# Performance work log

Hardware: AMD Instinct MI355X
Metric: run time of the kernel (lower is better)

Reference implementation:

```python
import jax, jax.numpy as jnp
import numpy as np

PATCH = 3
PAD = (PATCH - 1) // 2
WEIGHT = 100.0
EPS = 1e-9


def _extract_patches(fm):
    # fm: (C, H, W) -> (H*W, C*9) row i*W+j is the reflect-padded 3x3 patch at (i, j)
    C, H, W = fm.shape
    fm_pad = jnp.pad(fm, ((0, 0), (PAD, PAD), (PAD, PAD)), mode='reflect')
    shifts = [fm_pad[:, dh:dh + H, dw:dw + W] for dh in range(PATCH) for dw in range(PATCH)]
    p = jnp.stack(shifts, axis=0)            # (9, C, H, W)
    return p.reshape(PATCH * PATCH * C, H * W).T  # (HW, 9C)


def _match_fm(content_fm, style_fm):
    # content_fm, style_fm: (1, C, H, W); returns matched style fm (1,C,H,W) and idx (2,H,W)
    C, H, W = content_fm.shape[1:]
    cp = _extract_patches(content_fm[0])     # (HW, 9C) content patches (conv kernels)
    sp = _extract_patches(style_fm[0])       # (HW, 9C) style patches (conv sliding windows)
    c_norm = jnp.sqrt(jnp.sum(cp * cp, axis=1))  # kernel_norm per content location
    s_norm = jnp.sqrt(jnp.sum(sp * sp, axis=1))  # style_fm_norm per style location
    score = cp @ sp.T                            # (HW, HW) cross-correlation
    score = score / (c_norm[:, None] * s_norm[None, :] + EPS)
    idx = jnp.argmax(score, axis=1)              # flat argmax == torch.argmax on (H,W) map
    style_flat = style_fm[0].reshape(C, H * W)
    corr = style_flat[:, idx].reshape(1, C, H, W)  # gather matched style pixels
    corr_idx = jnp.stack([idx // W, idx % W], axis=0).reshape(2, H, W)
    return corr, corr_idx


def _masked_gram(fm, mask_flat, mask_sum):
    # fm: (1, C, H, W), mask_flat: (HW,) -> (C, C) gram of masked fm / sum(mask)
    C = fm.shape[1]
    f = fm[0].reshape(C, -1) * mask_flat[None, :]
    return (f @ f.T) / mask_sum


def setup_inputs() -> dict:
    key = jax.random.key(0)
    k1, k2, k3, k4 = jax.random.split(key, 4)
    B, C, H, W = 1, 512, 64, 64
    return {
        'content_fm': jax.random.normal(k1, (B, C, H, W), dtype=jnp.float32),
        'style_fm': jax.random.normal(k2, (B, C, H, W), dtype=jnp.float32),
        'input_fm': jax.random.normal(k3, (B, C, H, W), dtype=jnp.float32),
        'mask': jax.random.uniform(k4, (B, 1, H, W), dtype=jnp.float32),
    }


def reference(content_fm, style_fm, input_fm, mask):
    H, W = content_fm.shape[2:]
    mask_flat = mask[0, 0].reshape(H * W)
    mask_sum = jnp.sum(mask)
    # capture_style_ref: patch-match style fm to content fm, build target gram
    corr_fm, _ = _match_fm(content_fm, style_fm)
    target_gram = _masked_gram(corr_fm, mask_flat, mask_sum)
    # loss mode: masked gram of current image fm vs target, MSE (mean) * weight
    G = _masked_gram(input_fm, mask_flat, mask_sum)
    loss = jnp.mean((G - target_gram) ** 2) * WEIGHT
    return loss
```

## Files before the change

kernel.cpp:

```cpp
#include <hip/hip_runtime.h>

static constexpr int C  = 512;
static constexpr int P  = 4096;
static constexpr int CC = 262144;

typedef _Float16 half8  __attribute__((ext_vector_type(8)));
typedef _Float16 half2v __attribute__((ext_vector_type(2)));
typedef float    f32x4  __attribute__((ext_vector_type(4)));

__device__ __forceinline__ int refl(int q) { return q < 0 ? 1 : (q > 63 ? 62 : q); }

__device__ __forceinline__ void g2l16(const void* g, const void* l) {
    __builtin_amdgcn_global_load_lds((const __attribute__((address_space(1))) unsigned int*)g,
                                     (__attribute__((address_space(3))) unsigned int*)l, 16, 0, 0);
}

__global__ void k_init(float* __restrict__ small) {
    int e = blockIdx.x * 256 + threadIdx.x;
    if (e < 4096) small[e] = 0.0f;
    if (e == 0) small[8193] = 0.0f;
}

__global__ __launch_bounds__(256) void k_prep(const float* __restrict__ content, const float* __restrict__ style,
                                              _Float16* __restrict__ Ah, _Float16* __restrict__ Bh,
                                              float* __restrict__ sqn_s) {
    __shared__ float T[64][65];
    const int p0 = (blockIdx.x & 63) * 64, c0 = (blockIdx.x >> 6) * 64;
    const int pl = threadIdx.x & 63, cq = threadIdx.x >> 6;
    const int cl2 = threadIdx.x & 63, pq = threadIdx.x >> 6;

    #pragma unroll
    for (int r = 0; r < 16; ++r) {
        int cl = cq + r * 4;
        T[cl][pl] = content[(size_t)(c0 + cl) * P + p0 + pl];
    }
    __syncthreads();
    #pragma unroll
    for (int r = 0; r < 16; ++r) {
        int pl2 = pq + r * 4;
        Ah[(size_t)(p0 + pl2) * C + c0 + cl2] = (_Float16)T[cl2][pl2];
    }
    __syncthreads();

    float sq = 0.f;
    #pragma unroll
    for (int r = 0; r < 16; ++r) {
        int cl = cq + r * 4;
        float v = style[(size_t)(c0 + cl) * P + p0 + pl];
        T[cl][pl] = v;
        sq += v * v;
    }
    atomicAdd(&sqn_s[p0 + pl], sq);
    __syncthreads();
    #pragma unroll
    for (int r = 0; r < 16; ++r) {
        int pl2 = pq + r * 4;
        Bh[(size_t)(p0 + pl2) * C + c0 + cl2] = (_Float16)T[cl2][pl2];
    }
}

__global__ void k_pnorm(const float* __restrict__ sqn_s, const float* __restrict__ mask,
                        float* __restrict__ inv_sn, float* __restrict__ msum) {
    int p = blockIdx.x * 256 + threadIdx.x;
    int i = p >> 6, j = p & 63;
    float s2 = 0.f;
    #pragma unroll
    for (int dh = -1; dh <= 1; ++dh) {
        int ih = refl(i + dh);
        #pragma unroll
        for (int dw = -1; dw <= 1; ++dw)
            s2 += sqn_s[ih * 64 + refl(j + dw)];
    }
    inv_sn[p] = 1.0f / sqrtf(s2);

    if (blockIdx.x == 0) {
        __shared__ float red[256];
        float s = 0.f;
        for (int e = threadIdx.x; e < P; e += 256) s += mask[e];
        red[threadIdx.x] = s;
        __syncthreads();
        for (int t = 128; t > 0; t >>= 1) {
            if (threadIdx.x < t) red[threadIdx.x] += red[threadIdx.x + t];
            __syncthreads();
        }
        if (threadIdx.x == 0) msum[0] = red[0];
    }
}

__global__ __launch_bounds__(256) void k_gemm16(const _Float16* __restrict__ Ah,
                                                const _Float16* __restrict__ Bh,
                                                _Float16* __restrict__ Eo) {
    __shared__ _Float16 SH[16640];
    _Float16* As = SH;
    _Float16* Bs = SH + 8192;
    const int tid = threadIdx.x;
    const int wave = tid >> 6, lane = tid & 63;
    const int wr = wave >> 1, wc = wave & 1;
    const int quad = lane >> 4, l15 = lane & 15;
    const int i0 = blockIdx.y * 128, j0 = blockIdx.x * 128;

    int mloc[4], goff[4];
    #pragma unroll
    for (int c2 = 0; c2 < 4; ++c2) {
        int m = wave * 32 + c2 * 8 + (lane >> 3);
        mloc[c2] = m;
        goff[c2] = ((lane & 7) ^ (m & 7)) * 8;
    }

    int aoff[4][2], boff[4][2];
    #pragma unroll
    for (int mi = 0; mi < 4; ++mi) {
        int m = wr * 64 + mi * 16 + l15;
        int n = wc * 64 + mi * 16 + l15;
        #pragma unroll
        for (int kh = 0; kh < 2; ++kh) {
            aoff[mi][kh] = m * 64 + ((quad + kh * 4) ^ (m & 7)) * 8;
            boff[mi][kh] = n * 64 + ((quad + kh * 4) ^ (n & 7)) * 8;
        }
    }

    f32x4 acc[4][4] = {};

    for (int kk = 0; kk < C; kk += 64) {
        __syncthreads();
        #pragma unroll
        for (int c2 = 0; c2 < 4; ++c2) {
            g2l16(Ah + (size_t)(i0 + mloc[c2]) * C + kk + goff[c2], As + (wave * 32 + c2 * 8) * 64);
            g2l16(Bh + (size_t)(j0 + mloc[c2]) * C + kk + goff[c2], Bs + (wave * 32 + c2 * 8) * 64);
        }
        __syncthreads();
        half8 af[2][4], bf[2][4];
        #pragma unroll
        for (int kh = 0; kh < 2; ++kh)
            #pragma unroll
            for (int mi = 0; mi < 4; ++mi) {
                af[kh][mi] = *(const half8*)(As + aoff[mi][kh]);
                bf[kh][mi] = *(const half8*)(Bs + boff[mi][kh]);
            }
        #pragma unroll
        for (int kh = 0; kh < 2; ++kh)
            #pragma unroll
            for (int mi = 0; mi < 4; ++mi)
                #pragma unroll
                for (int ni = 0; ni < 4; ++ni)
                    acc[mi][ni] = __builtin_amdgcn_mfma_f32_16x16x32_f16(af[kh][mi], bf[kh][ni], acc[mi][ni], 0, 0, 0);
    }

    __syncthreads();
    #pragma unroll
    for (int mi = 0; mi < 4; ++mi) {
        int row = wr * 64 + mi * 16 + quad * 4;
        #pragma unroll
        for (int ni = 0; ni < 4; ++ni) {
            int col = wc * 64 + ni * 16 + l15;
            #pragma unroll
            for (int r = 0; r < 4; ++r)
                SH[(row + r) * 130 + col] = (_Float16)acc[mi][ni][r];
        }
    }
    __syncthreads();

    const int er  = tid >> 1;
    const int ec0 = (tid & 1) << 6;
    const int aw = er & 63;
    const int rm = (er & 64) | (aw == 0 ? 1 : aw - 1);
    const int rp = (er & 64) | (aw == 63 ? 62 : aw + 1);
    _Float16* outRow = Eo + (size_t)(i0 + er) * P + j0 + ec0;
    #pragma unroll
    for (int cc = 0; cc < 64; cc += 8) {
        half8 ev;
        #pragma unroll
        for (int u = 0; u < 8; ++u) {
            int c = ec0 + cc + u;
            int cw = c & 63;
            int cm = (c & 64) | (cw == 0 ? 1 : cw - 1);
            int cp = (c & 64) | (cw == 63 ? 62 : cw + 1);
            ev[u] = (_Float16)((float)SH[rm * 130 + cm] + (float)SH[er * 130 + c] + (float)SH[rp * 130 + cp]);
        }
        *(half8*)(outRow + cc) = ev;
    }
}

__global__ __launch_bounds__(256) void k_argmax(const _Float16* __restrict__ E,
                                                const float* __restrict__ inv_sn,
                                                int* __restrict__ idxOut) {
    const int i = blockIdx.x;
    const int ih = i >> 6, iw = i & 63;
    const int wave = threadIdx.x >> 6, l = threadIdx.x & 63, l15 = l & 15;
    size_t rb0 = (size_t)(refl(ih - 1) * 64 + iw) * P;
    size_t rb1 = (size_t)(ih * 64 + iw) * P;
    size_t rb2 = (size_t)(refl(ih + 1) * 64 + iw) * P;

    float best = -1e30f;
    int bidx = 0;
    #pragma unroll
    for (int s = 0; s < 4; ++s) {
        const int j0 = (wave * 4 + s) * 256 + l * 4;
        const int jh = j0 >> 6, jw0 = l15 * 4;
        const int cb0 = ((jh == 0) ? 1 : jh - 1) * 64 + jw0;
        const int cb1 = jh * 64 + jw0;
        const int cb2 = ((jh == 63) ? 62 : jh + 1) * 64 + jw0;
        uint2 u0 = *(const uint2*)(E + rb0 + cb0);
        uint2 u1 = *(const uint2*)(E + rb1 + cb1);
        uint2 u2 = *(const uint2*)(E + rb2 + cb2);
        half2v a0 = __builtin_bit_cast(half2v, u0.x), a1 = __builtin_bit_cast(half2v, u0.y);
        half2v b0 = __builtin_bit_cast(half2v, u1.x), b1 = __builtin_bit_cast(half2v, u1.y);
        half2v c0 = __builtin_bit_cast(half2v, u2.x), c1 = __builtin_bit_cast(half2v, u2.y);
        float f0 = (float)a0[0] + (float)b0[0] + (float)c0[0];
        float f1 = (float)a0[1] + (float)b0[1] + (float)c0[1];
        float f2 = (float)a1[0] + (float)b1[0] + (float)c1[0];
        float f3 = (float)a1[1] + (float)b1[1] + (float)c1[1];
        const float4 is = *(const float4*)(inv_sn + j0);
        float v0 = f0 * is.x, v1 = f1 * is.y, v2 = f2 * is.z, v3 = f3 * is.w;
        if (v0 > best) { best = v0; bidx = j0; }
        if (v1 > best) { best = v1; bidx = j0 + 1; }
        if (v2 > best) { best = v2; bidx = j0 + 2; }
        if (v3 > best) { best = v3; bidx = j0 + 3; }
    }

    __shared__ float bv[256];
    __shared__ int   bi[256];
    bv[threadIdx.x] = best;
    bi[threadIdx.x] = bidx;
    __syncthreads();
    for (int t = 128; t > 0; t >>= 1) {
        if (threadIdx.x < t) {
            float ov = bv[threadIdx.x + t];
            int   oi = bi[threadIdx.x + t];
            if (ov > bv[threadIdx.x] || (ov == bv[threadIdx.x] && oi < bi[threadIdx.x])) {
                bv[threadIdx.x] = ov;
                bi[threadIdx.x] = oi;
            }
        }
        __syncthreads();
    }
    if (threadIdx.x == 0) idxOut[i] = bi[0];
}

__global__ void k_build(const float* __restrict__ style, const float* __restrict__ input,
                        const float* __restrict__ mask, const int* __restrict__ idx,
                        _Float16* __restrict__ fc, _Float16* __restrict__ fg) {
    int t = blockIdx.x * 256 + threadIdx.x;
    int e0 = t * 8;
    int p0 = e0 & (P - 1), c = e0 >> 12;
    half8 vg, vc;
    #pragma unroll
    for (int u = 0; u < 8; ++u) {
        float m = mask[p0 + u];
        vg[u] = (_Float16)(input[e0 + u] * m);
        vc[u] = (_Float16)(style[(c << 12) + idx[p0 + u]] * m);
    }
    *(half8*)(fg + e0) = vg;
    *(half8*)(fc + e0) = vc;
}

__global__ __launch_bounds__(256) void k_gram(const _Float16* __restrict__ fg,
                                              const _Float16* __restrict__ fc,
                                              float* __restrict__ part) {
    const int z = blockIdx.z;
    const int p0 = z * 256;
    const int wave = threadIdx.x >> 6, lane = threadIdx.x & 63;
    const int wr = wave >> 1, wc = wave & 1, quad = lane >> 4, l15 = lane & 15;
    const int a0 = blockIdx.y * 128 + wr * 64, b0 = blockIdx.x * 128 + wc * 64;

    f32x4 accg[4][4] = {};
    f32x4 accc[4][4] = {};
    for (int ks = 0; ks < 256; ks += 32) {
        int kbase = p0 + ks + quad * 8;
        half8 af[4], bf[4];
        #pragma unroll
        for (int mi = 0; mi < 4; ++mi) af[mi] = *(const half8*)(fg + (size_t)(a0 + mi * 16 + l15) * P + kbase);
        #pragma unroll
        for (int ni = 0; ni < 4; ++ni) bf[ni] = *(const half8*)(fg + (size_t)(b0 + ni * 16 + l15) * P + kbase);
        #pragma unroll
        for (int mi = 0; mi < 4; ++mi)
            #pragma unroll
            for (int ni = 0; ni < 4; ++ni)
                accg[mi][ni] = __builtin_amdgcn_mfma_f32_16x16x32_f16(af[mi], bf[ni], accg[mi][ni], 0, 0, 0);
        #pragma unroll
        for (int mi = 0; mi < 4; ++mi) af[mi] = *(const half8*)(fc + (size_t)(a0 + mi * 16 + l15) * P + kbase);
        #pragma unroll
        for (int ni = 0; ni < 4; ++ni) bf[ni] = *(const half8*)(fc + (size_t)(b0 + ni * 16 + l15) * P + kbase);
        #pragma unroll
        for (int mi = 0; mi < 4; ++mi)
            #pragma unroll
            for (int ni = 0; ni < 4; ++ni)
                accc[mi][ni] = __builtin_amdgcn_mfma_f32_16x16x32_f16(af[mi], bf[ni], accc[mi][ni], 0, 0, 0);
    }
    #pragma unroll
    for (int mi = 0; mi < 4; ++mi)
        #pragma unroll
        for (int ni = 0; ni < 4; ++ni)
            #pragma unroll
            for (int r = 0; r < 4; ++r)
                part[(size_t)z * CC + (size_t)(a0 + mi * 16 + quad * 4 + r) * C + b0 + ni * 16 + l15]
                    = accg[mi][ni][r] - accc[mi][ni][r];
}

__global__ void k_loss(const float* __restrict__ part, float* __restrict__ acc) {
    int e = blockIdx.x * 256 + threadIdx.x;
    float d = 0.f;
    #pragma unroll
    for (int z = 0; z < 16; ++z) d += part[(size_t)z * CC + e];
    __shared__ float red[256];
    red[threadIdx.x] = d * d;
    __syncthreads();
    for (int t = 128; t > 0; t >>= 1) {
        if (threadIdx.x < t) red[threadIdx.x] += red[threadIdx.x + t];
        __syncthreads();
    }
    if (threadIdx.x == 0) atomicAdd(acc, red[0]);
}

__global__ void k_final(const float* __restrict__ msum, const float* __restrict__ acc,
                        float* __restrict__ out) {
    float m = msum[0];
    out[0] = acc[0] * 100.0f / (m * m * 262144.0f);
}

extern "C" void kernel_launch(void* const* d_in, const int* in_sizes, int n_in,
                              void* d_out, int out_size, void* d_ws, size_t ws_size,
                              hipStream_t stream) {
    (void)in_sizes; (void)n_in; (void)out_size; (void)ws_size;
    const float* content = (const float*)d_in[0];
    const float* style   = (const float*)d_in[1];
    const float* input   = (const float*)d_in[2];
    const float* mask    = (const float*)d_in[3];

    char* ws = (char*)d_ws;
    _Float16* Eb   = (_Float16*)ws;
    float*    part = (float*)ws;
    _Float16* Ah   = (_Float16*)(ws + (32u << 20));
    _Float16* Bh   = (_Float16*)(ws + (36u << 20));
    _Float16* fg_h = (_Float16*)(ws + (40u << 20));
    _Float16* fc_h = (_Float16*)(ws + (44u << 20));
    float*    small = (float*)(ws + (48u << 20));
    float* sqn_s  = small;
    float* inv_sn = small + 4096;
    float* msum   = small + 8192;
    float* acc    = small + 8193;
    int*   idx    = (int*)(small + 8194);
    float* out = (float*)d_out;

    k_init  <<<16, 256, 0, stream>>>(small);
    k_prep  <<<512, 256, 0, stream>>>(content, style, Ah, Bh, sqn_s);
    k_pnorm <<<16, 256, 0, stream>>>(sqn_s, mask, inv_sn, msum);
    k_gemm16<<<dim3(32, 32), 256, 0, stream>>>(Ah, Bh, Eb);
    k_argmax<<<4096, 256, 0, stream>>>(Eb, inv_sn, idx);
    k_build <<<1024, 256, 0, stream>>>(style, input, mask, idx, fc_h, fg_h);
    k_gram  <<<dim3(4, 4, 16), 256, 0, stream>>>(fg_h, fc_h, part);
    k_loss  <<<1024, 256, 0, stream>>>(part, acc);
    k_final <<<1, 1, 0, stream>>>(msum, acc, out);
}
```

Baseline: 173.1 us.

## Exploit Gram symmetry, drop atomics and init kernel, vectorize transposed stores

The Gram-difference kernel now computes only the 10 upper-triangular 128x128 tiles and weights off-diagonal tiles by two in the loss, cutting Gram MFMA work and partial-sum traffic by about 40%. Per-pixel style squared norms are written as per-channel-block partials and summed in k_pnorm, replacing atomics and the separate zero-init kernel. The loss reduction uses per-block partial sums reduced in k_final instead of an atomic. The transposed fp16 stores in k_prep become 16-byte vector writes.

```diff
diff --git a/kernel.cpp b/kernel.cpp
--- a/kernel.cpp
+++ b/kernel.cpp
@@ -2,7 +2,6 @@
 
 static constexpr int C  = 512;
 static constexpr int P  = 4096;
-static constexpr int CC = 262144;
 
 typedef _Float16 half8  __attribute__((ext_vector_type(8)));
 typedef _Float16 half2v __attribute__((ext_vector_type(2)));
@@ -15,65 +14,78 @@
                                      (__attribute__((address_space(3))) unsigned int*)l, 16, 0, 0);
 }
 
-__global__ void k_init(float* __restrict__ small) {
-    int e = blockIdx.x * 256 + threadIdx.x;
-    if (e < 4096) small[e] = 0.0f;
-    if (e == 0) small[8193] = 0.0f;
-}
-
 __global__ __launch_bounds__(256) void k_prep(const float* __restrict__ content, const float* __restrict__ style,
                                               _Float16* __restrict__ Ah, _Float16* __restrict__ Bh,
-                                              float* __restrict__ sqn_s) {
+                                              float* __restrict__ sqn_part) {
     __shared__ float T[64][65];
+    __shared__ float R4[4][64];
     const int p0 = (blockIdx.x & 63) * 64, c0 = (blockIdx.x >> 6) * 64;
     const int pl = threadIdx.x & 63, cq = threadIdx.x >> 6;
-    const int cl2 = threadIdx.x & 63, pq = threadIdx.x >> 6;
-
+    const int pv = threadIdx.x >> 3;
+    const int cv = (threadIdx.x & 7) * 8;
+
+    #pragma unroll
+    for (int r = 0; r < 16; ++r)
+        T[cq + r * 4][pl] = content[(size_t)(c0 + cq + r * 4) * P + p0 + pl];
+    __syncthreads();
+    #pragma unroll
+    for (int r = 0; r < 2; ++r) {
+        int pl2 = pv + r * 32;
+        half8 v;
+        #pragma unroll
+        for (int u = 0; u < 8; ++u) v[u] = (_Float16)T[cv + u][pl2];
+        *(half8*)(Ah + (size_t)(p0 + pl2) * C + c0 + cv) = v;
+    }
+    __syncthreads();
+
+    float sq = 0.f;
     #pragma unroll
     for (int r = 0; r < 16; ++r) {
-        int cl = cq + r * 4;
-        T[cl][pl] = content[(size_t)(c0 + cl) * P + p0 + pl];
-    }
-    __syncthreads();
-    #pragma unroll
-    for (int r = 0; r < 16; ++r) {
-        int pl2 = pq + r * 4;
-        Ah[(size_t)(p0 + pl2) * C + c0 + cl2] = (_Float16)T[cl2][pl2];
-    }
-    __syncthreads();
-
-    float sq = 0.f;
-    #pragma unroll
-    for (int r = 0; r < 16; ++r) {
-        int cl = cq + r * 4;
-        float v = style[(size_t)(c0 + cl) * P + p0 + pl];
-        T[cl][pl] = v;
+        float v = style[(size_t)(c0 + cq + r * 4) * P + p0 + pl];
+        T[cq + r * 4][pl] = v;
         sq += v * v;
     }
-    atomicAdd(&sqn_s[p0 + pl], sq);
-    __syncthreads();
-    #pragma unroll
-    for (int r = 0; r < 16; ++r) {
-        int pl2 = pq + r * 4;
-        Bh[(size_t)(p0 + pl2) * C + c0 + cl2] = (_Float16)T[cl2][pl2];
-    }
-}
-
-__global__ void k_pnorm(const float* __restrict__ sqn_s, const float* __restrict__ mask,
+    R4[cq][pl] = sq;
+    __syncthreads();
+    if (cq == 0)
+        sqn_part[(size_t)(blockIdx.x >> 6) * P + p0 + pl] = R4[0][pl] + R4[1][pl] + R4[2][pl] + R4[3][pl];
+    #pragma unroll
+    for (int r = 0; r < 2; ++r) {
+        int pl2 = pv + r * 32;
+        half8 v;
+        #pragma unroll
+        for (int u = 0; u < 8; ++u) v[u] = (_Float16)T[cv + u][pl2];
+        *(half8*)(Bh + (size_t)(p0 + pl2) * C + c0 + cv) = v;
+    }
+}
+
+__global__ void k_pnorm(const float* __restrict__ sqn_part, const float* __restrict__ mask,
                         float* __restrict__ inv_sn, float* __restrict__ msum) {
-    int p = blockIdx.x * 256 + threadIdx.x;
-    int i = p >> 6, j = p & 63;
+    __shared__ float sqs[6][64];
+    const int b = blockIdx.x;
+    for (int e = threadIdx.x; e < 384; e += 256) {
+        int rr = e >> 6, jw = e & 63;
+        int gr = refl(b * 4 - 1 + rr);
+        float s = 0.f;
+        #pragma unroll
+        for (int k = 0; k < 8; ++k) s += sqn_part[(size_t)k * P + gr * 64 + jw];
+        sqs[rr][jw] = s;
+    }
+    __syncthreads();
+
+    int p = b * 256 + threadIdx.x;
+    int li = (threadIdx.x >> 6) + 1;
+    int j = p & 63;
     float s2 = 0.f;
     #pragma unroll
     for (int dh = -1; dh <= 1; ++dh) {
-        int ih = refl(i + dh);
         #pragma unroll
         for (int dw = -1; dw <= 1; ++dw)
-            s2 += sqn_s[ih * 64 + refl(j + dw)];
+            s2 += sqs[li + dh][refl(j + dw)];
     }
     inv_sn[p] = 1.0f / sqrtf(s2);
 
-    if (blockIdx.x == 0) {
+    if (b == 0) {
         __shared__ float red[256];
         float s = 0.f;
         for (int e = threadIdx.x; e < P; e += 256) s += mask[e];
@@ -254,14 +266,17 @@
     *(half8*)(fc + e0) = vc;
 }
 
+__device__ __constant__ int TBX[10] = {0, 0, 1, 0, 1, 2, 0, 1, 2, 3};
+__device__ __constant__ int TBY[10] = {0, 1, 1, 2, 2, 2, 3, 3, 3, 3};
+
 __global__ __launch_bounds__(256) void k_gram(const _Float16* __restrict__ fg,
                                               const _Float16* __restrict__ fc,
                                               float* __restrict__ part) {
-    const int z = blockIdx.z;
+    const int t = blockIdx.x, z = blockIdx.z;
     const int p0 = z * 256;
     const int wave = threadIdx.x >> 6, lane = threadIdx.x & 63;
     const int wr = wave >> 1, wc = wave & 1, quad = lane >> 4, l15 = lane & 15;
-    const int a0 = blockIdx.y * 128 + wr * 64, b0 = blockIdx.x * 128 + wc * 64;
+    const int a0 = TBY[t] * 128 + wr * 64, b0 = TBX[t] * 128 + wc * 64;
 
     f32x4 accg[4][4] = {};
     f32x4 accc[4][4] = {};
@@ -287,35 +302,49 @@
             for (int ni = 0; ni < 4; ++ni)
                 accc[mi][ni] = __builtin_amdgcn_mfma_f32_16x16x32_f16(af[mi], bf[ni], accc[mi][ni], 0, 0, 0);
     }
+    float* dst = part + (size_t)(z * 10 + t) * 16384;
     #pragma unroll
     for (int mi = 0; mi < 4; ++mi)
         #pragma unroll
         for (int ni = 0; ni < 4; ++ni)
             #pragma unroll
             for (int r = 0; r < 4; ++r)
-                part[(size_t)z * CC + (size_t)(a0 + mi * 16 + quad * 4 + r) * C + b0 + ni * 16 + l15]
+                dst[(wr * 64 + mi * 16 + quad * 4 + r) * 128 + wc * 64 + ni * 16 + l15]
                     = accg[mi][ni][r] - accc[mi][ni][r];
 }
 
-__global__ void k_loss(const float* __restrict__ part, float* __restrict__ acc) {
+__global__ void k_loss(const float* __restrict__ part, float* __restrict__ lsum) {
     int e = blockIdx.x * 256 + threadIdx.x;
+    int t = e >> 14, loc = e & 16383;
     float d = 0.f;
     #pragma unroll
-    for (int z = 0; z < 16; ++z) d += part[(size_t)z * CC + e];
+    for (int z = 0; z < 16; ++z) d += part[(size_t)(z * 10 + t) * 16384 + loc];
+    float w = (TBX[t] == TBY[t]) ? 1.0f : 2.0f;
     __shared__ float red[256];
-    red[threadIdx.x] = d * d;
+    red[threadIdx.x] = d * d * w;
+    __syncthreads();
+    for (int s = 128; s > 0; s >>= 1) {
+        if (threadIdx.x < s) red[threadIdx.x] += red[threadIdx.x + s];
+        __syncthreads();
+    }
+    if (threadIdx.x == 0) lsum[blockIdx.x] = red[0];
+}
+
+__global__ void k_final(const float* __restrict__ lsum, const float* __restrict__ msum,
+                        float* __restrict__ out) {
+    __shared__ float red[256];
+    float s = 0.f;
+    for (int e = threadIdx.x; e < 640; e += 256) s += lsum[e];
+    red[threadIdx.x] = s;
     __syncthreads();
     for (int t = 128; t > 0; t >>= 1) {
         if (threadIdx.x < t) red[threadIdx.x] += red[threadIdx.x + t];
         __syncthreads();
     }
-    if (threadIdx.x == 0) atomicAdd(acc, red[0]);
-}
-
-__global__ void k_final(const float* __restrict__ msum, const float* __restrict__ acc,
-                        float* __restrict__ out) {
-    float m = msum[0];
-    out[0] = acc[0] * 100.0f / (m * m * 262144.0f);
+    if (threadIdx.x == 0) {
+        float m = msum[0];
+        out[0] = red[0] * 100.0f / (m * m * 262144.0f);
+    }
 }
 
 extern "C" void kernel_launch(void* const* d_in, const int* in_sizes, int n_in,
@@ -335,20 +364,19 @@
     _Float16* fg_h = (_Float16*)(ws + (40u << 20));
     _Float16* fc_h = (_Float16*)(ws + (44u << 20));
     float*    small = (float*)(ws + (48u << 20));
-    float* sqn_s  = small;
-    float* inv_sn = small + 4096;
-    float* msum   = small + 8192;
-    float* acc    = small + 8193;
-    int*   idx    = (int*)(small + 8194);
+    float* sqn_part = small;
+    float* inv_sn   = small + 32768;
+    float* msum     = small + 36864;
+    float* lsum     = small + 36992;
+    int*   idx      = (int*)(small + 37888);
     float* out = (float*)d_out;
 
-    k_init  <<<16, 256, 0, stream>>>(small);
-    k_prep  <<<512, 256, 0, stream>>>(content, style, Ah, Bh, sqn_s);
-    k_pnorm <<<16, 256, 0, stream>>>(sqn_s, mask, inv_sn, msum);
+    k_prep  <<<512, 256, 0, stream>>>(content, style, Ah, Bh, sqn_part);
+    k_pnorm <<<16, 256, 0, stream>>>(sqn_part, mask, inv_sn, msum);
     k_gemm16<<<dim3(32, 32), 256, 0, stream>>>(Ah, Bh, Eb);
     k_argmax<<<4096, 256, 0, stream>>>(Eb, inv_sn, idx);
     k_build <<<1024, 256, 0, stream>>>(style, input, mask, idx, fc_h, fg_h);
-    k_gram  <<<dim3(4, 4, 16), 256, 0, stream>>>(fg_h, fc_h, part);
-    k_loss  <<<1024, 256, 0, stream>>>(part, acc);
-    k_final <<<1, 1, 0, stream>>>(msum, acc, out);
-}
+    k_gram  <<<dim3(10, 1, 16), 256, 0, stream>>>(fg_h, fc_h, part);
+    k_loss  <<<640, 256, 0, stream>>>(part, lsum);
+    k_final <<<1, 256, 0, stream>>>(lsum, msum, out);
+}
```

After: 155.4 us. 10.2% less time.
